# Optimization experiments

Measured on AMD Instinct MI355X. Metric: run time of the kernel, lower is better.

Reference implementation:

```python
import jax, jax.numpy as jnp
import numpy as np

MIN_BIN_WIDTH = 1e-3
MIN_BIN_HEIGHT = 1e-3
MIN_DERIVATIVE = 1e-3
TAIL_BOUND = 10.0
EPS = 1e-6  # matches nflows searchsorted eps on the last bin edge
B, D, K = 32768, 512, 10


def setup_inputs() -> dict:
    key = jax.random.key(0)
    k1, k2, k3, k4 = jax.random.split(key, 4)
    return {
        # scale so some elements fall outside the +/- tail_bound linear tails
        "x": jax.random.normal(k1, (B, D), jnp.float32) * 4.0,
        "unnormalized_widths": jax.random.uniform(k2, (D, K), jnp.float32),
        "unnormalized_heights": jax.random.uniform(k3, (D, K), jnp.float32),
        "unnormalized_derivatives": jax.random.uniform(k4, (D, K - 1), jnp.float32),
    }


def _rqs_forward(x, uw, uh, ud):
    """Unconstrained rational-quadratic spline, forward direction.
    x: [B, D]; uw/uh: [D, K]; ud: [D, K-1]. Params shared across batch.
    Returns (y [B, D], logdet [B]).
    """
    left = -TAIL_BOUND
    right = TAIL_BOUND

    # normalized bin widths / cumulative x-knots  [D, K] / [D, K+1]
    w = jax.nn.softmax(uw, axis=-1)
    w = MIN_BIN_WIDTH + (1.0 - MIN_BIN_WIDTH * K) * w
    cw = jnp.concatenate([jnp.zeros((D, 1), w.dtype), jnp.cumsum(w, -1)], -1)
    cw = (right - left) * cw + left
    cw = cw.at[:, 0].set(left).at[:, -1].set(right)
    w = cw[:, 1:] - cw[:, :-1]

    # normalized bin heights / cumulative y-knots
    h = jax.nn.softmax(uh, axis=-1)
    h = MIN_BIN_HEIGHT + (1.0 - MIN_BIN_HEIGHT * K) * h
    ch = jnp.concatenate([jnp.zeros((D, 1), h.dtype), jnp.cumsum(h, -1)], -1)
    ch = (right - left) * ch + left
    ch = ch.at[:, 0].set(left).at[:, -1].set(right)
    h = ch[:, 1:] - ch[:, :-1]

    # boundary derivatives padded with softplus^{-1}(1 - min_derivative)
    const = np.log(np.exp(1.0 - MIN_DERIVATIVE) - 1.0).astype(np.float32)
    pad = jnp.full((D, 1), const, ud.dtype)
    d = MIN_DERIVATIVE + jax.nn.softplus(jnp.concatenate([pad, ud, pad], -1))  # [D, K+1]

    inside = (x >= left) & (x <= right)
    xc = jnp.clip(x, left, right)  # tails handled by identity below

    # per-element bin search (last edge bumped by EPS, as in nflows)
    cw_s = cw.at[:, -1].add(EPS)
    idx = jnp.sum(xc[..., None] >= cw_s[None], axis=-1) - 1  # [B, D]
    idx = jnp.clip(idx, 0, K - 1)

    feat = jnp.arange(D)[None, :]  # broadcast with idx [B, D]
    in_cw = cw[feat, idx]
    in_w = w[feat, idx]
    in_ch = ch[feat, idx]
    in_h = h[feat, idx]
    delta = h / w
    in_delta = delta[feat, idx]
    in_d = d[feat, idx]
    in_dp1 = d[feat, idx + 1]

    theta = (xc - in_cw) / in_w
    t1m = theta * (1.0 - theta)
    numerator = in_h * (in_delta * theta**2 + in_d * t1m)
    denominator = in_delta + (in_d + in_dp1 - 2.0 * in_delta) * t1m
    y = in_ch + numerator / denominator

    deriv_num = in_delta**2 * (in_dp1 * theta**2 + 2.0 * in_delta * t1m + in_d * (1.0 - theta) ** 2)
    lad = jnp.log(deriv_num) - 2.0 * jnp.log(denominator)

    y = jnp.where(inside, y, x)          # linear tails: identity
    lad = jnp.where(inside, lad, 0.0)    # logabsdet 0 in tails
    return y, jnp.sum(lad, axis=1)


def reference(x, unnormalized_widths, unnormalized_heights, unnormalized_derivatives):
    return _rqs_forward(x, unnormalized_widths, unnormalized_heights, unnormalized_derivatives)
```

## Files before the change

### kernel.cpp

```cpp
#include <hip/hip_runtime.h>

#define NB 32768
#define ND 512
#define NK 10

#define LEFTB (-10.0f)
#define RIGHTB (10.0f)
#define ROWS 8
#define BX 512
#define FPB 128

#define OFF_CWCH (9 * ND)
#define OFF_DD   (OFF_CWCH + 22 * ND)
#define OFF_PART (OFF_DD + 11 * ND)

__global__ void rqs_precompute(const float* __restrict__ uw,
                               const float* __restrict__ uh,
                               const float* __restrict__ ud,
                               float* __restrict__ ws) {
    int f = blockIdx.x * blockDim.x + threadIdx.x;
    if (f >= ND) return;

    float* E = ws;
    float2* GCWCH = (float2*)(ws + OFF_CWCH);
    float* GDD = ws + OFF_DD;

    float cw[NK + 1], ch[NK + 1], dd[NK + 1];

    {
        float u[NK];
        float m = -1e30f;
#pragma unroll
        for (int k = 0; k < NK; ++k) { u[k] = uw[f * NK + k]; m = fmaxf(m, u[k]); }
        float s = 0.0f;
#pragma unroll
        for (int k = 0; k < NK; ++k) { u[k] = expf(u[k] - m); s += u[k]; }
        float inv = 1.0f / s;
        float c = 0.0f;
        cw[0] = LEFTB;
#pragma unroll
        for (int k = 0; k < NK; ++k) {
            float wk = 1e-3f + (1.0f - 1e-3f * NK) * (u[k] * inv);
            c += wk;
            cw[k + 1] = (RIGHTB - LEFTB) * c + LEFTB;
        }
        cw[NK] = RIGHTB;
    }
    {
        float u[NK];
        float m = -1e30f;
#pragma unroll
        for (int k = 0; k < NK; ++k) { u[k] = uh[f * NK + k]; m = fmaxf(m, u[k]); }
        float s = 0.0f;
#pragma unroll
        for (int k = 0; k < NK; ++k) { u[k] = expf(u[k] - m); s += u[k]; }
        float inv = 1.0f / s;
        float c = 0.0f;
        ch[0] = LEFTB;
#pragma unroll
        for (int k = 0; k < NK; ++k) {
            float hk = 1e-3f + (1.0f - 1e-3f * NK) * (u[k] * inv);
            c += hk;
            ch[k + 1] = (RIGHTB - LEFTB) * c + LEFTB;
        }
        ch[NK] = RIGHTB;
    }
    dd[0] = 1.0f;
    dd[NK] = 1.0f;
#pragma unroll
    for (int k = 1; k < NK; ++k) {
        float v = ud[f * (NK - 1) + (k - 1)];
        dd[k] = 1e-3f + (fmaxf(v, 0.0f) + log1pf(expf(-fabsf(v))));
    }

#pragma unroll
    for (int j = 0; j < 9; ++j) E[j * ND + f] = cw[j + 1];
#pragma unroll
    for (int k = 0; k <= NK; ++k) {
        GCWCH[k * ND + f] = make_float2(cw[k], ch[k]);
        GDD[k * ND + f] = dd[k];
    }
}

__device__ __forceinline__ float dpp_row_reduce16(float v) {
    v += __int_as_float(__builtin_amdgcn_update_dpp(
        0, __float_as_int(v), 0x111, 0xF, 0xF, true));
    v += __int_as_float(__builtin_amdgcn_update_dpp(
        0, __float_as_int(v), 0x112, 0xF, 0xF, true));
    v += __int_as_float(__builtin_amdgcn_update_dpp(
        0, __float_as_int(v), 0x114, 0xF, 0xF, true));
    v += __int_as_float(__builtin_amdgcn_update_dpp(
        0, __float_as_int(v), 0x118, 0xF, 0xF, true));
    return v;
}

__global__ __launch_bounds__(128) void rqs_main(const float* __restrict__ X,
                                                const float* __restrict__ ws,
                                                float* __restrict__ Y,
                                                float* __restrict__ part) {
    const int t = threadIdx.x;
    const int q = blockIdx.y;
    const int f = q * FPB + t;

    const float* E = ws;
    const float2* GCWCH = (const float2*)(ws + OFF_CWCH);
    const float* GDD = ws + OFF_DD;

    __shared__ float2 sCWCH[NK + 1][FPB];
    __shared__ float sDD[NK + 1][FPB];

#pragma unroll
    for (int k = 0; k <= NK; ++k) {
        sCWCH[k][t] = GCWCH[k * ND + f];
        sDD[k][t] = GDD[k * ND + f];
    }
    float e[9];
#pragma unroll
    for (int j = 0; j < 9; ++j) e[j] = E[j * ND + f];
    __syncthreads();

    const int step = gridDim.x * ROWS;

    for (int r0 = blockIdx.x * ROWS; r0 < NB; r0 += step) {
        float xs[ROWS], ys[ROWS], ls[ROWS];
#pragma unroll
        for (int i = 0; i < ROWS; ++i)
            xs[i] = __builtin_nontemporal_load(&X[(r0 + i) * ND + f]);

#pragma unroll
        for (int i = 0; i < ROWS; ++i) {
            float x = xs[i];

            int idx = 0;
#pragma unroll
            for (int j = 0; j < 9; ++j) idx += (x >= e[j]) ? 1 : 0;

            float2 c0 = sCWCH[idx][t];
            float2 c1 = sCWCH[idx + 1][t];
            float dk = sDD[idx][t];
            float dk1 = sDD[idx + 1][t];

            float w = c1.x - c0.x;
            float rw = __builtin_amdgcn_rcpf(w);
            float h = c1.y - c0.y;
            float delta = h * rw;

            float theta = (x - c0.x) * rw;
            float omt = 1.0f - theta;
            float t1m = theta * omt;
            float th2 = theta * theta;

            float num = h * fmaf(delta, th2, dk * t1m);
            float den = fmaf(fmaf(-2.0f, delta, dk + dk1), t1m, delta);
            float rden = __builtin_amdgcn_rcpf(den);
            float y = fmaf(num, rden, c0.y);

            float dnum = delta * delta *
                         (fmaf(dk1, th2, 2.0f * delta * t1m) + dk * omt * omt);
            float lad2 = __log2f(dnum * rden * rden);

            bool inside = fabsf(x) <= RIGHTB;
            ys[i] = inside ? y : x;
            ls[i] = inside ? lad2 : 0.0f;
        }

#pragma unroll
        for (int i = 0; i < ROWS; ++i)
            __builtin_nontemporal_store(ys[i], &Y[(r0 + i) * ND + f]);

#pragma unroll
        for (int i = 0; i < ROWS; ++i) ls[i] = dpp_row_reduce16(ls[i]);
        if ((t & 15) == 15) {
            int g = q * 8 + (t >> 4);
#pragma unroll
            for (int i = 0; i < ROWS; ++i) part[(r0 + i) * 32 + g] = ls[i];
        }
    }
}

__global__ __launch_bounds__(256) void rqs_reduce(const float* __restrict__ part,
                                                  float* __restrict__ logdet) {
    int j = blockIdx.x * 256 + threadIdx.x;
    int row = j >> 3;
    int sub = j & 7;
    float4 v = ((const float4*)part)[row * 8 + sub];
    float s = (v.x + v.y) + (v.z + v.w);
    s += __shfl_xor(s, 1, 64);
    s += __shfl_xor(s, 2, 64);
    s += __shfl_xor(s, 4, 64);
    if (sub == 0) logdet[row] = s * 0.6931471805599453f;
}

extern "C" void kernel_launch(void* const* d_in, const int* in_sizes, int n_in,
                              void* d_out, int out_size, void* d_ws, size_t ws_size,
                              hipStream_t stream) {
    const float* x  = (const float*)d_in[0];
    const float* uw = (const float*)d_in[1];
    const float* uh = (const float*)d_in[2];
    const float* ud = (const float*)d_in[3];

    float* out = (float*)d_out;
    float* Y = out;
    float* logdet = out + (size_t)NB * ND;

    float* ws = (float*)d_ws;
    float* part = ws + OFF_PART;

    hipLaunchKernelGGL(rqs_precompute, dim3(4), dim3(128), 0, stream,
                       uw, uh, ud, ws);
    hipLaunchKernelGGL(rqs_main, dim3(BX, 4), dim3(128), 0, stream,
                       x, ws, Y, part);
    hipLaunchKernelGGL(rqs_reduce, dim3(NB * 8 / 256), dim3(256), 0, stream,
                       part, logdet);
}
```

Measured before the change: 45.92 us.

## Fuse logdet reduction into main kernel with full-row 512-thread blocks

Each block now covers all 512 features of a row instead of a quarter, so the per-row logdet sum can be finished in shared memory inside the main kernel. This removes the separate reduce kernel launch and the global partial-sum buffer round trip. In exchange it adds two block-wide barriers per 8-row iteration and uses larger blocks with more shared memory, which may lower occupancy and stall the memory stream.

```diff
diff --git a/kernel.cpp b/kernel.cpp
--- a/kernel.cpp
+++ b/kernel.cpp
@@ -7,12 +7,10 @@
 #define LEFTB (-10.0f)
 #define RIGHTB (10.0f)
 #define ROWS 8
-#define BX 512
-#define FPB 128
+#define NBLK 512
 
 #define OFF_CWCH (9 * ND)
 #define OFF_DD   (OFF_CWCH + 22 * ND)
-#define OFF_PART (OFF_DD + 11 * ND)
 
 __global__ void rqs_precompute(const float* __restrict__ uw,
                                const float* __restrict__ uh,
@@ -40,8 +38,7 @@
         cw[0] = LEFTB;
 #pragma unroll
         for (int k = 0; k < NK; ++k) {
-            float wk = 1e-3f + (1.0f - 1e-3f * NK) * (u[k] * inv);
-            c += wk;
+            c += 1e-3f + (1.0f - 1e-3f * NK) * (u[k] * inv);
             cw[k + 1] = (RIGHTB - LEFTB) * c + LEFTB;
         }
         cw[NK] = RIGHTB;
@@ -59,8 +56,7 @@
         ch[0] = LEFTB;
 #pragma unroll
         for (int k = 0; k < NK; ++k) {
-            float hk = 1e-3f + (1.0f - 1e-3f * NK) * (u[k] * inv);
-            c += hk;
+            c += 1e-3f + (1.0f - 1e-3f * NK) * (u[k] * inv);
             ch[k + 1] = (RIGHTB - LEFTB) * c + LEFTB;
         }
         ch[NK] = RIGHTB;
@@ -70,7 +66,7 @@
 #pragma unroll
     for (int k = 1; k < NK; ++k) {
         float v = ud[f * (NK - 1) + (k - 1)];
-        dd[k] = 1e-3f + (fmaxf(v, 0.0f) + log1pf(expf(-fabsf(v))));
+        dd[k] = 1e-3f + fmaxf(v, 0.0f) + log1pf(expf(-fabsf(v)));
     }
 
 #pragma unroll
@@ -94,38 +90,35 @@
     return v;
 }
 
-__global__ __launch_bounds__(128) void rqs_main(const float* __restrict__ X,
+__global__ __launch_bounds__(512) void rqs_main(const float* __restrict__ X,
                                                 const float* __restrict__ ws,
                                                 float* __restrict__ Y,
-                                                float* __restrict__ part) {
+                                                float* __restrict__ logdet) {
     const int t = threadIdx.x;
-    const int q = blockIdx.y;
-    const int f = q * FPB + t;
+
+    __shared__ float2 sCWCH[NK + 1][ND];
+    __shared__ float sDD[NK + 1][ND];
+    __shared__ float sPart[ROWS][32];
 
     const float* E = ws;
     const float2* GCWCH = (const float2*)(ws + OFF_CWCH);
     const float* GDD = ws + OFF_DD;
 
-    __shared__ float2 sCWCH[NK + 1][FPB];
-    __shared__ float sDD[NK + 1][FPB];
-
 #pragma unroll
     for (int k = 0; k <= NK; ++k) {
-        sCWCH[k][t] = GCWCH[k * ND + f];
-        sDD[k][t] = GDD[k * ND + f];
+        sCWCH[k][t] = GCWCH[k * ND + t];
+        sDD[k][t] = GDD[k * ND + t];
     }
     float e[9];
 #pragma unroll
-    for (int j = 0; j < 9; ++j) e[j] = E[j * ND + f];
+    for (int j = 0; j < 9; ++j) e[j] = E[j * ND + t];
     __syncthreads();
 
-    const int step = gridDim.x * ROWS;
-
-    for (int r0 = blockIdx.x * ROWS; r0 < NB; r0 += step) {
+    for (int r0 = blockIdx.x * ROWS; r0 < NB; r0 += NBLK * ROWS) {
         float xs[ROWS], ys[ROWS], ls[ROWS];
 #pragma unroll
         for (int i = 0; i < ROWS; ++i)
-            xs[i] = __builtin_nontemporal_load(&X[(r0 + i) * ND + f]);
+            xs[i] = __builtin_nontemporal_load(&X[(r0 + i) * ND + t]);
 
 #pragma unroll
         for (int i = 0; i < ROWS; ++i) {
@@ -166,29 +159,29 @@
 
 #pragma unroll
         for (int i = 0; i < ROWS; ++i)
-            __builtin_nontemporal_store(ys[i], &Y[(r0 + i) * ND + f]);
+            __builtin_nontemporal_store(ys[i], &Y[(r0 + i) * ND + t]);
 
 #pragma unroll
         for (int i = 0; i < ROWS; ++i) ls[i] = dpp_row_reduce16(ls[i]);
         if ((t & 15) == 15) {
-            int g = q * 8 + (t >> 4);
-#pragma unroll
-            for (int i = 0; i < ROWS; ++i) part[(r0 + i) * 32 + g] = ls[i];
-        }
-    }
-}
-
-__global__ __launch_bounds__(256) void rqs_reduce(const float* __restrict__ part,
-                                                  float* __restrict__ logdet) {
-    int j = blockIdx.x * 256 + threadIdx.x;
-    int row = j >> 3;
-    int sub = j & 7;
-    float4 v = ((const float4*)part)[row * 8 + sub];
-    float s = (v.x + v.y) + (v.z + v.w);
-    s += __shfl_xor(s, 1, 64);
-    s += __shfl_xor(s, 2, 64);
-    s += __shfl_xor(s, 4, 64);
-    if (sub == 0) logdet[row] = s * 0.6931471805599453f;
+            int g = t >> 4;
+#pragma unroll
+            for (int i = 0; i < ROWS; ++i) sPart[i][g] = ls[i];
+        }
+        __syncthreads();
+
+        if (t < 256) {
+            float v = ((const float*)sPart)[t];
+            v += __shfl_xor(v, 1, 32);
+            v += __shfl_xor(v, 2, 32);
+            v += __shfl_xor(v, 4, 32);
+            v += __shfl_xor(v, 8, 32);
+            v += __shfl_xor(v, 16, 32);
+            if ((t & 31) == 0)
+                logdet[r0 + (t >> 5)] = v * 0.6931471805599453f;
+        }
+        __syncthreads();
+    }
 }
 
 extern "C" void kernel_launch(void* const* d_in, const int* in_sizes, int n_in,
@@ -204,12 +197,9 @@
     float* logdet = out + (size_t)NB * ND;
 
     float* ws = (float*)d_ws;
-    float* part = ws + OFF_PART;
 
     hipLaunchKernelGGL(rqs_precompute, dim3(4), dim3(128), 0, stream,
                        uw, uh, ud, ws);
-    hipLaunchKernelGGL(rqs_main, dim3(BX, 4), dim3(128), 0, stream,
-                       x, ws, Y, part);
-    hipLaunchKernelGGL(rqs_reduce, dim3(NB * 8 / 256), dim3(256), 0, stream,
-                       part, logdet);
-}
+    hipLaunchKernelGGL(rqs_main, dim3(NBLK), dim3(ND), 0, stream,
+                       x, ws, Y, logdet);
+}
```

Measured after the change: 43.06 us. -6.2%, faster.

## Use 1024-thread blocks covering all features and prefetch next rows

Applied to the files above, without the earlier changes.

The main kernel now launches 512 blocks of 1024 threads. Each block covers all 512 features across two row-halves of 8 rows, where before it used 128-feature blocks on a 2D grid. The row loop software-prefetches the next sweep's X values into registers while computing the current ones. Spline tables are loaded into shared memory once per block, with the two halves of the block splitting the load. The change is meant to hide load latency and cut the per-block table-loading overhead, at the cost of more shared memory and registers per block. This could reduce occupancy under the (1024, 8) launch bounds.

```diff
diff --git a/kernel.cpp b/kernel.cpp
--- a/kernel.cpp
+++ b/kernel.cpp
@@ -7,8 +7,8 @@
 #define LEFTB (-10.0f)
 #define RIGHTB (10.0f)
 #define ROWS 8
-#define BX 512
-#define FPB 128
+#define NBLK 512
+#define SWEEPS (NB / (NBLK * 16))
 
 #define OFF_CWCH (9 * ND)
 #define OFF_DD   (OFF_CWCH + 22 * ND)
@@ -40,8 +40,7 @@
         cw[0] = LEFTB;
 #pragma unroll
         for (int k = 0; k < NK; ++k) {
-            float wk = 1e-3f + (1.0f - 1e-3f * NK) * (u[k] * inv);
-            c += wk;
+            c += 1e-3f + (1.0f - 1e-3f * NK) * (u[k] * inv);
             cw[k + 1] = (RIGHTB - LEFTB) * c + LEFTB;
         }
         cw[NK] = RIGHTB;
@@ -59,8 +58,7 @@
         ch[0] = LEFTB;
 #pragma unroll
         for (int k = 0; k < NK; ++k) {
-            float hk = 1e-3f + (1.0f - 1e-3f * NK) * (u[k] * inv);
-            c += hk;
+            c += 1e-3f + (1.0f - 1e-3f * NK) * (u[k] * inv);
             ch[k + 1] = (RIGHTB - LEFTB) * c + LEFTB;
         }
         ch[NK] = RIGHTB;
@@ -70,7 +68,7 @@
 #pragma unroll
     for (int k = 1; k < NK; ++k) {
         float v = ud[f * (NK - 1) + (k - 1)];
-        dd[k] = 1e-3f + (fmaxf(v, 0.0f) + log1pf(expf(-fabsf(v))));
+        dd[k] = 1e-3f + fmaxf(v, 0.0f) + log1pf(expf(-fabsf(v)));
     }
 
 #pragma unroll
@@ -94,39 +92,53 @@
     return v;
 }
 
-__global__ __launch_bounds__(128) void rqs_main(const float* __restrict__ X,
-                                                const float* __restrict__ ws,
-                                                float* __restrict__ Y,
-                                                float* __restrict__ part) {
+__global__ __launch_bounds__(1024, 8) void rqs_main(const float* __restrict__ X,
+                                                    const float* __restrict__ ws,
+                                                    float* __restrict__ Y,
+                                                    float* __restrict__ part) {
     const int t = threadIdx.x;
-    const int q = blockIdx.y;
-    const int f = q * FPB + t;
+    const int fl = t & (ND - 1);
+    const int hf = t >> 9;
+
+    __shared__ float2 sCWCH[NK + 1][ND];
+    __shared__ float sDD[NK + 1][ND];
 
     const float* E = ws;
     const float2* GCWCH = (const float2*)(ws + OFF_CWCH);
     const float* GDD = ws + OFF_DD;
 
-    __shared__ float2 sCWCH[NK + 1][FPB];
-    __shared__ float sDD[NK + 1][FPB];
-
-#pragma unroll
-    for (int k = 0; k <= NK; ++k) {
-        sCWCH[k][t] = GCWCH[k * ND + f];
-        sDD[k][t] = GDD[k * ND + f];
+    if (hf == 0) {
+#pragma unroll
+        for (int k = 0; k <= NK; ++k) sCWCH[k][fl] = GCWCH[k * ND + fl];
+    } else {
+#pragma unroll
+        for (int k = 0; k <= NK; ++k) sDD[k][fl] = GDD[k * ND + fl];
     }
     float e[9];
 #pragma unroll
-    for (int j = 0; j < 9; ++j) e[j] = E[j * ND + f];
+    for (int j = 0; j < 9; ++j) e[j] = E[j * ND + fl];
     __syncthreads();
 
-    const int step = gridDim.x * ROWS;
-
-    for (int r0 = blockIdx.x * ROWS; r0 < NB; r0 += step) {
-        float xs[ROWS], ys[ROWS], ls[ROWS];
+    float xs[ROWS];
+    {
+        const int rb = blockIdx.x * 16 + hf * ROWS;
 #pragma unroll
         for (int i = 0; i < ROWS; ++i)
-            xs[i] = __builtin_nontemporal_load(&X[(r0 + i) * ND + f]);
-
+            xs[i] = __builtin_nontemporal_load(&X[(rb + i) * ND + fl]);
+    }
+
+    for (int it = 0; it < SWEEPS; ++it) {
+        const int rb = blockIdx.x * 16 + it * (NBLK * 16) + hf * ROWS;
+
+        float xn[ROWS];
+        if (it + 1 < SWEEPS) {
+            const int rn = rb + NBLK * 16;
+#pragma unroll
+            for (int i = 0; i < ROWS; ++i)
+                xn[i] = __builtin_nontemporal_load(&X[(rn + i) * ND + fl]);
+        }
+
+        float ls[ROWS];
 #pragma unroll
         for (int i = 0; i < ROWS; ++i) {
             float x = xs[i];
@@ -135,10 +147,10 @@
 #pragma unroll
             for (int j = 0; j < 9; ++j) idx += (x >= e[j]) ? 1 : 0;
 
-            float2 c0 = sCWCH[idx][t];
-            float2 c1 = sCWCH[idx + 1][t];
-            float dk = sDD[idx][t];
-            float dk1 = sDD[idx + 1][t];
+            float2 c0 = sCWCH[idx][fl];
+            float2 c1 = sCWCH[idx + 1][fl];
+            float dk = sDD[idx][fl];
+            float dk1 = sDD[idx + 1][fl];
 
             float w = c1.x - c0.x;
             float rw = __builtin_amdgcn_rcpf(w);
@@ -160,21 +172,18 @@
             float lad2 = __log2f(dnum * rden * rden);
 
             bool inside = fabsf(x) <= RIGHTB;
-            ys[i] = inside ? y : x;
-            ls[i] = inside ? lad2 : 0.0f;
-        }
-
-#pragma unroll
-        for (int i = 0; i < ROWS; ++i)
-            __builtin_nontemporal_store(ys[i], &Y[(r0 + i) * ND + f]);
-
-#pragma unroll
-        for (int i = 0; i < ROWS; ++i) ls[i] = dpp_row_reduce16(ls[i]);
+            __builtin_nontemporal_store(inside ? y : x, &Y[(rb + i) * ND + fl]);
+            ls[i] = dpp_row_reduce16(inside ? lad2 : 0.0f);
+        }
+
         if ((t & 15) == 15) {
-            int g = q * 8 + (t >> 4);
-#pragma unroll
-            for (int i = 0; i < ROWS; ++i) part[(r0 + i) * 32 + g] = ls[i];
-        }
+            int g = fl >> 4;
+#pragma unroll
+            for (int i = 0; i < ROWS; ++i) part[(rb + i) * 32 + g] = ls[i];
+        }
+
+#pragma unroll
+        for (int i = 0; i < ROWS; ++i) xs[i] = xn[i];
     }
 }
 
@@ -208,7 +217,7 @@
 
     hipLaunchKernelGGL(rqs_precompute, dim3(4), dim3(128), 0, stream,
                        uw, uh, ud, ws);
-    hipLaunchKernelGGL(rqs_main, dim3(BX, 4), dim3(128), 0, stream,
+    hipLaunchKernelGGL(rqs_main, dim3(NBLK), dim3(1024), 0, stream,
                        x, ws, Y, part);
     hipLaunchKernelGGL(rqs_reduce, dim3(NB * 8 / 256), dim3(256), 0, stream,
                        part, logdet);
```

After: 44.56 us. -3.0%, faster.
